# Kernel optimization log

Measured on AMD Instinct MI355X. Metric: run time of the kernel, lower is better.

The kernel has to match this reference:

```python
import jax, jax.numpy as jnp
import numpy as np
from jax import lax

TAU = 2.0
NUM_HEADS = 8
EPS = 1e-5
ALPHA = 4.0  # surrogate sigmoid sharpness

@jax.custom_vjp
def heaviside(x):
    # torch.heaviside(x, 1.0): 1 for x >= 0 (value 1 at x==0), 0 for x < 0
    return (x >= 0).astype(x.dtype)

def _hv_fwd(x):
    return (x >= 0).astype(x.dtype), x

def _hv_bwd(x, g):
    s = jax.nn.sigmoid(x * ALPHA)
    return (g * s * (1.0 - s) * ALPHA,)

heaviside.defvjp(_hv_fwd, _hv_bwd)

def lif(x):
    # Leaky-integrate-fire recurrence over leading time axis. x: [T, ...]
    def step(v, xt):
        v = v + (xt - v) / TAU                 # leakage
        s = heaviside(v - 1.0)                 # fire (v_threshold = 1.0)
        v = (1.0 - lax.stop_gradient(s)) * v   # hard reset (detached spike)
        return v, s
    _, spikes = lax.scan(step, jnp.zeros_like(x[0]), x)
    return spikes

def conv1x1(x, w):
    # x: [T,B,Cin,H,W], w: [Cout,Cin] (1x1 conv, no bias)
    return jnp.einsum('tbchw,dc->tbdhw', x, w)

def bn(x, gamma, beta, mean, var):
    # BatchNorm2d in eval mode (running stats), per-channel over axis 2
    shp = (1, 1, -1, 1, 1)
    inv = gamma.reshape(shp) / jnp.sqrt(var.reshape(shp) + EPS)
    return (x - mean.reshape(shp)) * inv + beta.reshape(shp)

def setup_inputs():
    key = jax.random.key(0)
    ks = jax.random.split(key, 10)
    T, B, C, H, W = 4, 32, 256, 16, 16
    Cv = C  # lamda_ratio = 1

    def w_init(k, o, i):
        return jax.random.normal(k, (o, i), jnp.float32) * (1.0 / np.sqrt(i))

    def bn_params(k, c):
        k1, k2, k3, k4 = jax.random.split(k, 4)
        gamma = jax.random.uniform(k1, (c,), jnp.float32, 0.5, 1.5)
        beta = jax.random.normal(k2, (c,), jnp.float32) * 0.1
        mean = jax.random.normal(k3, (c,), jnp.float32) * 0.1
        var = jax.random.uniform(k4, (c,), jnp.float32, 0.5, 1.5)
        return gamma, beta, mean, var

    x = jax.random.normal(ks[0], (T, B, C, H, W), jnp.float32)
    q_w = w_init(ks[1], C, C)
    k_w = w_init(ks[2], C, C)
    v_w = w_init(ks[3], Cv, C)
    proj_w = w_init(ks[4], C, Cv)
    q_gamma, q_beta, q_mean, q_var = bn_params(ks[5], C)
    k_gamma, k_beta, k_mean, k_var = bn_params(ks[6], C)
    v_gamma, v_beta, v_mean, v_var = bn_params(ks[7], Cv)
    p_gamma, p_beta, p_mean, p_var = bn_params(ks[8], C)
    return {
        'x': x,
        'q_w': q_w, 'q_gamma': q_gamma, 'q_beta': q_beta, 'q_mean': q_mean, 'q_var': q_var,
        'k_w': k_w, 'k_gamma': k_gamma, 'k_beta': k_beta, 'k_mean': k_mean, 'k_var': k_var,
        'v_w': v_w, 'v_gamma': v_gamma, 'v_beta': v_beta, 'v_mean': v_mean, 'v_var': v_var,
        'proj_w': proj_w, 'p_gamma': p_gamma, 'p_beta': p_beta, 'p_mean': p_mean, 'p_var': p_var,
    }

def reference(x, q_w, q_gamma, q_beta, q_mean, q_var,
              k_w, k_gamma, k_beta, k_mean, k_var,
              v_w, v_gamma, v_beta, v_mean, v_var,
              proj_w, p_gamma, p_beta, p_mean, p_var):
    T, B, C, H, W = x.shape
    N = H * W
    Cv = v_w.shape[0]
    hd = C // NUM_HEADS
    hdv = Cv // NUM_HEADS
    scale = (C // NUM_HEADS) ** -0.5

    xs = lif(x)  # head_spike

    q = lif(bn(conv1x1(xs, q_w), q_gamma, q_beta, q_mean, q_var))  # [T,B,C,H,W] binary
    k = lif(bn(conv1x1(xs, k_w), k_gamma, k_beta, k_mean, k_var))
    v = lif(bn(conv1x1(xs, v_w), v_gamma, v_beta, v_mean, v_var))  # [T,B,Cv,H,W]

    # channel c = h*hd + d; flatten spatial -> tokens N, split heads
    q = q.reshape(T, B, NUM_HEADS, hd, N).transpose(0, 1, 2, 4, 3)   # [T,B,h,N,d]
    k = k.reshape(T, B, NUM_HEADS, hd, N).transpose(0, 1, 2, 4, 3)
    v = v.reshape(T, B, NUM_HEADS, hdv, N).transpose(0, 1, 2, 4, 3)  # [T,B,h,N,dv]

    attn = jnp.einsum('tbhnd,tbhmd->tbhnm', q, k)                    # QK^T
    out = jnp.einsum('tbhnm,tbhmd->tbhnd', attn, v) * (scale * 2.0)  # (QK^T)V * 2*scale

    out = out.transpose(0, 1, 2, 4, 3).reshape(T, B, Cv, N)          # [T,B,Cv,N]
    out = lif(out)                                                   # attn_spike
    out = out.reshape(T, B, Cv, H, W)
    out = bn(conv1x1(out, proj_w), p_gamma, p_beta, p_mean, p_var)   # [T,B,C,H,W]
    return out
```

## Files before the change

### kernel.cpp

```cpp
#include <hip/hip_runtime.h>

#define TT 4
#define BB 32
#define CC 256
#define NN 256
#define EPSf 1e-5f
#define MULTf 0.35355339059327373f
#define MARGINQ 1e-2f
#define BCAP 8192u

typedef __attribute__((ext_vector_type(8))) short s16x8;
typedef __attribute__((ext_vector_type(4))) float f32x4;
typedef unsigned char uchar;
typedef unsigned int uint;
typedef unsigned short ushort;

__device__ __forceinline__ ushort f2bf_rn(float f) {
  uint u = __float_as_uint(f);
  u = (u + 0x7FFFu + ((u >> 16) & 1u)) >> 16;
  return (ushort)u;
}
__device__ __forceinline__ float bf2f(ushort b) {
  return __uint_as_float(((uint)b) << 16);
}

__global__ __launch_bounds__(256) void k_front(
    const float* __restrict__ x, uchar* __restrict__ xsF, uchar* __restrict__ xsP,
    const float* __restrict__ qw, const float* __restrict__ kw,
    const float* __restrict__ vw, const float* __restrict__ pw,
    const float* __restrict__ qga, const float* __restrict__ qva,
    const float* __restrict__ kga, const float* __restrict__ kva,
    const float* __restrict__ vga, const float* __restrict__ vva,
    uchar* __restrict__ wfq, uchar* __restrict__ wfp, uint* __restrict__ flags) {
  const int tid = threadIdx.x;
  const int bid = blockIdx.x;
  if (bid < 256) {
#pragma clang fp contract(off)
    const int b = bid >> 3;
    const int ksq = bid & 7;
    const int oct = tid >> 6;
    const int nq = tid & 63;
    const int c0 = ksq * 32 + oct * 8;
    const int n0 = nq * 4;
    const size_t stride = (size_t)BB * CC * NN;
    const float* xb = x + ((size_t)b * CC + c0) * NN + n0;

    float v[8][4];
#pragma unroll
    for (int j = 0; j < 8; ++j)
#pragma unroll
      for (int nn = 0; nn < 4; ++nn) v[j][nn] = 0.f;

#pragma unroll
    for (int t = 0; t < TT; ++t) {
      ushort sp[8][4];
      uint pm[4] = {0, 0, 0, 0};
#pragma unroll
      for (int j = 0; j < 8; ++j) {
        const float4 xv = *reinterpret_cast<const float4*>(xb + t * stride + (size_t)j * NN);
        const float xa[4] = {xv.x, xv.y, xv.z, xv.w};
#pragma unroll
        for (int nn = 0; nn < 4; ++nn) {
          float d = (xa[nn] - v[j][nn]) * 0.5f;
          v[j][nn] = v[j][nn] + d;
          bool s = (v[j][nn] >= 1.0f);
          sp[j][nn] = s ? (ushort)0x3F80 : (ushort)0;
          if (s) { v[j][nn] = 0.f; pm[nn] |= 1u << j; }
        }
      }
#pragma unroll
      for (int nn = 0; nn < 4; ++nn) {
        const int n = n0 + nn;
        uint4* dst = reinterpret_cast<uint4*>(xsF) +
                     (((size_t)(t * BB + b) * 16 + (n >> 4)) * 512 + ksq * 64 + oct * 16 + (n & 15));
        uint4 o;
        o.x = (uint)sp[0][nn] | ((uint)sp[1][nn] << 16);
        o.y = (uint)sp[2][nn] | ((uint)sp[3][nn] << 16);
        o.z = (uint)sp[4][nn] | ((uint)sp[5][nn] << 16);
        o.w = (uint)sp[6][nn] | ((uint)sp[7][nn] << 16);
        *dst = o;
        xsP[(((size_t)(t * BB + b) * NN + n) << 5) + ksq * 4 + oct] = (uchar)pm[nn];
      }
    }
  } else {
    const int gid = (bid - 256) * 256 + tid;
    if (gid < 256) flags[gid] = 0;
    const int ob2 = gid >> 9;
    const int e = gid & 511;
    const int ks = e >> 6, l = e & 63;
    const int c0 = ks * 32 + (l >> 4) * 8;
    if (ob2 < 48) {
      const int sel = ob2 >> 4;
      const float* Wb = sel == 0 ? qw : (sel == 1 ? kw : vw);
      const float* G = sel == 0 ? qga : (sel == 1 ? kga : vga);
      const float* Vr = sel == 0 ? qva : (sel == 1 ? kva : vva);
      const int ocr = (ob2 & 15) * 16 + (l & 15);
      const float inv = G[ocr] / sqrtf(Vr[ocr] + EPSf);
      const float* W = Wb + (size_t)ocr * CC;
      float wv[8];
      *reinterpret_cast<float4*>(&wv[0]) = *reinterpret_cast<const float4*>(W + c0);
      *reinterpret_cast<float4*>(&wv[4]) = *reinterpret_cast<const float4*>(W + c0 + 4);
      ushort hi[8];
#pragma unroll
      for (int j = 0; j < 8; ++j) hi[j] = f2bf_rn(wv[j] * inv);
      *reinterpret_cast<uint4*>(wfq + (((size_t)ob2 * 8 + ks) * 64 + l) * 16) =
          *reinterpret_cast<const uint4*>(hi);
    } else {
      const int ob = ob2 - 48;
      const float* W = pw + ((size_t)(ob * 16 + (l & 15))) * CC;
      float wv[8];
      *reinterpret_cast<float4*>(&wv[0]) = *reinterpret_cast<const float4*>(W + c0);
      *reinterpret_cast<float4*>(&wv[4]) = *reinterpret_cast<const float4*>(W + c0 + 4);
      ushort hi[8], lo[8];
#pragma unroll
      for (int j = 0; j < 8; ++j) {
        hi[j] = f2bf_rn(wv[j]);
        lo[j] = f2bf_rn(wv[j] - bf2f(hi[j]));
      }
      const size_t base = (((size_t)ob * 8 + ks) * 64 + l) * 16;
      const size_t sstr = (size_t)16 * 8 * 64 * 16;
      *reinterpret_cast<uint4*>(wfp + base) = *reinterpret_cast<const uint4*>(hi);
      *reinterpret_cast<uint4*>(wfp + sstr + base) = *reinterpret_cast<const uint4*>(lo);
    }
  }
}

__global__ __launch_bounds__(256, 2) void k_qkv_mfma(
    const uchar* __restrict__ xsF, const uchar* __restrict__ wfq,
    const float* __restrict__ qga, const float* __restrict__ qbe, const float* __restrict__ qme, const float* __restrict__ qva,
    const float* __restrict__ kga, const float* __restrict__ kbe, const float* __restrict__ kme, const float* __restrict__ kva,
    const float* __restrict__ vga, const float* __restrict__ vbe, const float* __restrict__ vme, const float* __restrict__ vva,
    ushort* __restrict__ qp, uint* __restrict__ flags) {
  const int tid = threadIdx.x;
  const int wc = tid >> 6, lane = tid & 63;
  const int lhi = lane >> 4, llo = lane & 15;
  const int bid = blockIdx.x;
  const int xcd = bid & 7;
  const int r0 = bid >> 3;
  const int j = r0 % 12;
  const int g = (r0 / 12) * 8 + xcd;
  const int b = g >> 2, ntile = g & 3;
  const int oc0 = j * 64;
  const int sel = j >> 2;
  const float* G  = sel == 0 ? qga : (sel == 1 ? kga : vga);
  const float* Be = sel == 0 ? qbe : (sel == 1 ? kbe : vbe);
  const float* Mn = sel == 0 ? qme : (sel == 1 ? kme : vme);
  const float* Vr = sel == 0 ? qva : (sel == 1 ? kva : vva);

  s16x8 wfr[4][8];
#pragma unroll
  for (int mf = 0; mf < 4; ++mf)
#pragma unroll
    for (int ks = 0; ks < 8; ++ks)
      wfr[mf][ks] = *reinterpret_cast<const s16x8*>(
          wfq + (((size_t)(j * 4 + mf) * 8 + ks) * 64 + lane) * 16);

  float bias8[4][4];
#pragma unroll
  for (int mf = 0; mf < 4; ++mf)
#pragma unroll
    for (int rr = 0; rr < 4; ++rr) {
      const int ocb = (j & 3) * 64 + mf * 16 + lhi * 4 + rr;
      const float inv = G[ocb] / sqrtf(Vr[ocb] + EPSf);
      bias8[mf][rr] = Be[ocb] - Mn[ocb] * inv;
    }

  float vst[4][4];
#pragma unroll
  for (int mf = 0; mf < 4; ++mf)
#pragma unroll
    for (int rr = 0; rr < 4; ++rr) vst[mf][rr] = 0.f;
  uint fl = 0;
  ushort qm[TT][4];
  const int nb = ntile * 4 + wc;

#define BPTR(t_, ks_)                                                   \
  reinterpret_cast<const s16x8*>(                                       \
      xsF + ((((size_t)((t_) * BB + b) * 16 + nb) * 512 + (ks_) * 64 + lane) * 16))

  s16x8 bfr[8];
#pragma unroll
  for (int ks = 0; ks < 8; ++ks) bfr[ks] = *BPTR(0, ks);

#pragma unroll
  for (int t = 0; t < TT; ++t) {
    f32x4 acc[4];
#pragma unroll
    for (int mf = 0; mf < 4; ++mf) acc[mf] = (f32x4){0.f, 0.f, 0.f, 0.f};

#pragma unroll
    for (int ks = 0; ks < 8; ++ks) {
#pragma unroll
      for (int mf = 0; mf < 4; ++mf)
        acc[mf] = __builtin_amdgcn_mfma_f32_16x16x32_bf16(wfr[mf][ks], bfr[ks], acc[mf], 0, 0, 0);
      if (t < TT - 1) bfr[ks] = *BPTR(t + 1, ks);
    }

#pragma unroll
    for (int mf = 0; mf < 4; ++mf)
#pragma unroll
      for (int rr = 0; rr < 4; ++rr) {
        float y = acc[mf][rr] + bias8[mf][rr];
        float v = vst[mf][rr];
        v = v + (y - v) * 0.5f;
        const bool sp = (v >= 1.0f);
        if (fabsf(v - 1.0f) < MARGINQ) fl |= 1u << (mf * 4 + rr);
        const unsigned long long m = __ballot(sp);
        if (llo == rr) qm[t][mf] = (ushort)((m >> (lhi * 16)) & 0xFFFFull);
        vst[mf][rr] = sp ? 0.f : v;
      }
  }
#undef BPTR

  if (llo < 4) {
#pragma unroll
    for (int t = 0; t < TT; ++t) {
      ushort* qrow = qp + (size_t)(t * BB + b) * 768 * 16;
#pragma unroll
      for (int mf = 0; mf < 4; ++mf) {
        const int oc = oc0 + mf * 16 + lhi * 4 + llo;
        qrow[(size_t)oc * 16 + ntile * 4 + wc] = qm[t][mf];
      }
    }
  }

  if (fl) {
#pragma unroll
    for (int mf = 0; mf < 4; ++mf)
#pragma unroll
      for (int rr = 0; rr < 4; ++rr)
        if (fl & (1u << (mf * 4 + rr))) {
          const int oc = oc0 + mf * 16 + lhi * 4 + rr;
          const int n = ntile * 64 + wc * 16 + llo;
          const uint bucket = ((uint)b << 3) | (uint)((oc & 255) >> 5);
          const uint idx = atomicAdd(&flags[bucket], 1u);
          if (idx < BCAP)
            flags[256 + (bucket << 13) + idx] =
                (((uint)(b << 10) | (uint)oc) << 8) | (uint)n;
        }
  }
}

__global__ __launch_bounds__(256) void k_fix(
    const uchar* __restrict__ xsP,
    const float* __restrict__ qw, const float* __restrict__ kw, const float* __restrict__ vw,
    const float* __restrict__ qga, const float* __restrict__ qbe, const float* __restrict__ qme, const float* __restrict__ qva,
    const float* __restrict__ kga, const float* __restrict__ kbe, const float* __restrict__ kme, const float* __restrict__ kva,
    const float* __restrict__ vga, const float* __restrict__ vbe, const float* __restrict__ vme, const float* __restrict__ vva,
    uint* __restrict__ qp32, const uint* __restrict__ flags) {
#pragma clang fp contract(off)
  const uint bucket = blockIdx.x;
  const int b = (int)(bucket >> 3);
  const uint cnt = min(flags[bucket], BCAP);
  for (uint i = threadIdx.x; i < cnt; i += 256) {
    const uint e = flags[256 + (bucket << 13) + i];
    const int n = (int)(e & 255);
    const int oc = (int)((e >> 8) & 1023);
    const int sel = oc >> 8, ocl = oc & 255;
    const float* W = (sel == 0 ? qw : (sel == 1 ? kw : vw)) + (size_t)ocl * CC;
    const float* G  = sel == 0 ? qga : (sel == 1 ? kga : vga);
    const float* Be = sel == 0 ? qbe : (sel == 1 ? kbe : vbe);
    const float* Mn = sel == 0 ? qme : (sel == 1 ? kme : vme);
    const float* Vr = sel == 0 ? qva : (sel == 1 ? kva : vva);

    uint bw[4][8];
#pragma unroll
    for (int t = 0; t < TT; ++t) {
      const uint4* p = reinterpret_cast<const uint4*>(
          xsP + (((size_t)(t * BB + b) * NN + n) << 5));
      uint4 a = p[0], c4 = p[1];
      bw[t][0] = a.x;  bw[t][1] = a.y;  bw[t][2] = a.z;  bw[t][3] = a.w;
      bw[t][4] = c4.x; bw[t][5] = c4.y; bw[t][6] = c4.z; bw[t][7] = c4.w;
    }

    const float4* W4 = reinterpret_cast<const float4*>(W);
    float a0 = 0.f, a1 = 0.f, a2 = 0.f, a3 = 0.f;
#pragma unroll
    for (int gg = 0; gg < 32; ++gg) {
      const float4 w0 = W4[2 * gg];
      const float4 w1 = W4[2 * gg + 1];
      const uint s0 = bw[0][gg >> 2] >> ((gg & 3) * 8);
      const uint s1 = bw[1][gg >> 2] >> ((gg & 3) * 8);
      const uint s2 = bw[2][gg >> 2] >> ((gg & 3) * 8);
      const uint s3 = bw[3][gg >> 2] >> ((gg & 3) * 8);
      const float wv[8] = {w0.x, w0.y, w0.z, w0.w, w1.x, w1.y, w1.z, w1.w};
#pragma unroll
      for (int jj = 0; jj < 8; ++jj) {
        a0 = fmaf(wv[jj], (float)((s0 >> jj) & 1u), a0);
        a1 = fmaf(wv[jj], (float)((s1 >> jj) & 1u), a1);
        a2 = fmaf(wv[jj], (float)((s2 >> jj) & 1u), a2);
        a3 = fmaf(wv[jj], (float)((s3 >> jj) & 1u), a3);
      }
    }
    float accs[4] = {a0, a1, a2, a3};

    const float inv = G[ocl] / sqrtf(Vr[ocl] + EPSf);
    const float mean = Mn[ocl], beta = Be[ocl];
    float v = 0.f;
#pragma unroll
    for (int t = 0; t < TT; ++t) {
      float xm = accs[t] - mean;
      float y = xm * inv;
      y = y + beta;
      float d = (y - v) * 0.5f;
      v = v + d;
      const bool sp = (v >= 1.0f);
      const size_t widx = ((size_t)(t * BB + b) * 768 + oc) * 8 + (n >> 5);
      const uint bit = 1u << (n & 31);
      if (sp) atomicOr(&qp32[widx], bit);
      else atomicAnd(&qp32[widx], ~bit);
      if (sp) v = 0.f;
    }
  }
}

__global__ __launch_bounds__(1024) void k_attn(const ushort* __restrict__ qp,
                                               uchar* __restrict__ attnF) {
  __shared__ uint Qb[32][8], Kb[32][8], Vb[32][8];
  __shared__ ushort KtVT[32][40];
  const int tid = threadIdx.x;
  const int b = blockIdx.x >> 3;
  const int h = blockIdx.x & 7;
  const int lane = tid & 63;
  const int nt = tid >> 6;
  const int l15 = lane & 15, lhi = lane >> 4;
  const int n = nt * 16 + l15;
  const int wq = n >> 5, bitn = n & 31;

  float vst[8];
#pragma unroll
  for (int j = 0; j < 8; ++j) vst[j] = 0.f;

  for (int t = 0; t < TT; ++t) {
    __syncthreads();
    const ushort* base = qp + (size_t)(t * BB + b) * 768 * 16;
    if (tid < 768) {
      const int arr = tid >> 8;
      const int idx = tid & 255;
      const int ch = idx >> 3, wv2 = idx & 7;
      const uint val = *reinterpret_cast<const uint*>(
          base + (size_t)(arr * 256 + h * 32 + ch) * 16 + wv2 * 2);
      uint(*dst)[8] = (arr == 0) ? Qb : (arr == 1) ? Kb : Vb;
      dst[ch][wv2] = val;
    }
    __syncthreads();
    {
      const int ii = tid >> 5, jj = tid & 31;
      int s = 0;
#pragma unroll
      for (int w8 = 0; w8 < 8; ++w8) s += __popc(Kb[ii][w8] & Vb[jj][w8]);
      KtVT[jj][ii] = f2bf_rn((float)s);
    }
    __syncthreads();

    s16x8 bq;
#pragma unroll
    for (int k = 0; k < 8; ++k) {
      const uint qwv = Qb[lhi * 8 + k][wq];
      bq[k] = (short)(((qwv >> bitn) & 1u) ? 0x3F80 : 0);
    }
    s16x8 a0 = *reinterpret_cast<const s16x8*>(&KtVT[l15][lhi * 8]);
    s16x8 a1 = *reinterpret_cast<const s16x8*>(&KtVT[16 + l15][lhi * 8]);
    f32x4 acc0 = (f32x4){0.f, 0.f, 0.f, 0.f};
    f32x4 acc1 = (f32x4){0.f, 0.f, 0.f, 0.f};
    acc0 = __builtin_amdgcn_mfma_f32_16x16x32_bf16(a0, bq, acc0, 0, 0, 0);
    acc1 = __builtin_amdgcn_mfma_f32_16x16x32_bf16(a1, bq, acc1, 0, 0, 0);

    ushort sb[8];
    {
#pragma clang fp contract(off)
#pragma unroll
      for (int mt = 0; mt < 2; ++mt)
#pragma unroll
        for (int r = 0; r < 4; ++r) {
          const float av = (mt == 0) ? acc0[r] : acc1[r];
          float y = av * MULTf;
          float v = vst[mt * 4 + r];
          float d = (y - v) * 0.5f;
          v = v + d;
          const bool sp = (v >= 1.0f);
          sb[mt * 4 + r] = sp ? (ushort)0x3F80 : (ushort)0;
          vst[mt * 4 + r] = sp ? 0.f : v;
        }
    }
#pragma unroll
    for (int mt = 0; mt < 2; ++mt) {
      uint2 o;
      o.x = (uint)sb[mt * 4 + 0] | ((uint)sb[mt * 4 + 1] << 16);
      o.y = (uint)sb[mt * 4 + 2] | ((uint)sb[mt * 4 + 3] << 16);
      const int oct2 = mt * 2 + (lhi >> 1);
      uchar* dst = attnF +
                   ((((size_t)(t * BB + b) * 16 + nt) * 512 + h * 64 + oct2 * 16 + l15) * 16) +
                   (lhi & 1) * 8;
      *reinterpret_cast<uint2*>(dst) = o;
    }
  }
}

__global__ __launch_bounds__(256, 4) void k_proj_mfma(
    const uchar* __restrict__ attnF, const uchar* __restrict__ wfp,
    const float* __restrict__ pga, const float* __restrict__ pbe,
    const float* __restrict__ pme, const float* __restrict__ pva,
    float* __restrict__ out) {
  const int tid = threadIdx.x;
  const int w = tid >> 6, lane = tid & 63;
  const int lhi = lane >> 4, llo = lane & 15;
  const int wr = w >> 1, wc = w & 1;
  const int bid = blockIdx.x;
  const int xcd = bid & 7;
  const int r = bid >> 3;
  const int j = r & 3;
  const int g = (r >> 2) * 8 + xcd;
  const int tb = g >> 2, ntile = g & 3;
  const int oc0 = j * 64;
  const int nb0 = ntile * 4 + wc * 2;

  f32x4 acc[2][2];
#pragma unroll
  for (int mf = 0; mf < 2; ++mf)
#pragma unroll
    for (int nf = 0; nf < 2; ++nf) acc[mf][nf] = (f32x4){0.f, 0.f, 0.f, 0.f};

#pragma unroll
  for (int ks = 0; ks < 8; ++ks) {
    s16x8 wf[2][2];
#pragma unroll
    for (int s = 0; s < 2; ++s)
#pragma unroll
      for (int mf = 0; mf < 2; ++mf) {
        const int ob = j * 4 + wr * 2 + mf;
        wf[s][mf] = *reinterpret_cast<const s16x8*>(
            wfp + ((((size_t)s * 16 + ob) * 8 + ks) * 64 + lane) * 16);
      }
    s16x8 bf0 = *reinterpret_cast<const s16x8*>(
        attnF + ((((size_t)tb * 16 + nb0) * 512 + ks * 64 + lane) * 16));
    s16x8 bf1 = *reinterpret_cast<const s16x8*>(
        attnF + ((((size_t)tb * 16 + nb0 + 1) * 512 + ks * 64 + lane) * 16));
#pragma unroll
    for (int s = 0; s < 2; ++s)
#pragma unroll
      for (int mf = 0; mf < 2; ++mf) {
        acc[mf][0] = __builtin_amdgcn_mfma_f32_16x16x32_bf16(wf[s][mf], bf0, acc[mf][0], 0, 0, 0);
        acc[mf][1] = __builtin_amdgcn_mfma_f32_16x16x32_bf16(wf[s][mf], bf1, acc[mf][1], 0, 0, 0);
      }
  }

  float inv8[2][4], mean8[2][4], beta8[2][4];
#pragma unroll
  for (int mf = 0; mf < 2; ++mf)
#pragma unroll
    for (int rr = 0; rr < 4; ++rr) {
      const int ocb = oc0 + wr * 32 + mf * 16 + lhi * 4 + rr;
      inv8[mf][rr] = pga[ocb] / sqrtf(pva[ocb] + EPSf);
      mean8[mf][rr] = pme[ocb];
      beta8[mf][rr] = pbe[ocb];
    }

#pragma unroll
  for (int mf = 0; mf < 2; ++mf)
#pragma unroll
    for (int nf = 0; nf < 2; ++nf)
#pragma unroll
      for (int rr = 0; rr < 4; ++rr) {
        const int oc = oc0 + wr * 32 + mf * 16 + lhi * 4 + rr;
        const int nn = ntile * 64 + wc * 32 + nf * 16 + llo;
        float y = (acc[mf][nf][rr] - mean8[mf][rr]) * inv8[mf][rr] + beta8[mf][rr];
        out[((size_t)tb * CC + oc) * NN + nn] = y;
      }
}

extern "C" void kernel_launch(void* const* d_in, const int* in_sizes, int n_in,
                              void* d_out, int out_size, void* d_ws, size_t ws_size,
                              hipStream_t stream) {
  const float* x = (const float*)d_in[0];
  const float* q_w = (const float*)d_in[1];
  const float* q_g = (const float*)d_in[2];
  const float* q_b = (const float*)d_in[3];
  const float* q_m = (const float*)d_in[4];
  const float* q_v = (const float*)d_in[5];
  const float* k_w = (const float*)d_in[6];
  const float* k_g = (const float*)d_in[7];
  const float* k_b = (const float*)d_in[8];
  const float* k_m = (const float*)d_in[9];
  const float* k_v = (const float*)d_in[10];
  const float* v_w = (const float*)d_in[11];
  const float* v_g = (const float*)d_in[12];
  const float* v_b = (const float*)d_in[13];
  const float* v_m = (const float*)d_in[14];
  const float* v_v = (const float*)d_in[15];
  const float* p_w = (const float*)d_in[16];
  const float* p_g = (const float*)d_in[17];
  const float* p_b = (const float*)d_in[18];
  const float* p_m = (const float*)d_in[19];
  const float* p_v = (const float*)d_in[20];

  uchar* ws = (uchar*)d_ws;
  uchar* xsF  = ws;
  ushort* qp  = (ushort*)(ws + 16777216);
  uchar* wfq  = ws + 19922944;
  uchar* wfp  = ws + 20447232;
  uchar* xsP  = ws + 20971520;
  uint* flags = (uint*)(ws + 22020096);

  k_front<<<dim3(384), 256, 0, stream>>>(x, xsF, xsP, q_w, k_w, v_w, p_w,
                                         q_g, q_v, k_g, k_v, v_g, v_v,
                                         wfq, wfp, flags);
  k_qkv_mfma<<<dim3(1536), 256, 0, stream>>>(xsF, wfq,
                                             q_g, q_b, q_m, q_v,
                                             k_g, k_b, k_m, k_v,
                                             v_g, v_b, v_m, v_v,
                                             qp, flags);
  k_fix<<<dim3(256), 256, 0, stream>>>(xsP, q_w, k_w, v_w,
                                       q_g, q_b, q_m, q_v,
                                       k_g, k_b, k_m, k_v,
                                       v_g, v_b, v_m, v_v,
                                       (uint*)qp, flags);
  k_attn<<<dim3(256), 1024, 0, stream>>>(qp, xsF );
  k_proj_mfma<<<dim3(2048), 256, 0, stream>>>(xsF, wfp, p_g, p_b, p_m, p_v,
                                              (float*)d_out);
}
```

Before: 96.75 us.

## Fuse near-threshold fp32 recompute fixup into QKV MFMA kernel via LDS list

```diff
diff --git a/kernel.cpp b/kernel.cpp
--- a/kernel.cpp
+++ b/kernel.cpp
@@ -7,7 +7,7 @@
 #define EPSf 1e-5f
 #define MULTf 0.35355339059327373f
 #define MARGINQ 1e-2f
-#define BCAP 8192u
+#define FCAP 2048u
 
 typedef __attribute__((ext_vector_type(8))) short s16x8;
 typedef __attribute__((ext_vector_type(4))) float f32x4;
@@ -31,7 +31,7 @@
     const float* __restrict__ qga, const float* __restrict__ qva,
     const float* __restrict__ kga, const float* __restrict__ kva,
     const float* __restrict__ vga, const float* __restrict__ vva,
-    uchar* __restrict__ wfq, uchar* __restrict__ wfp, uint* __restrict__ flags) {
+    uchar* __restrict__ wfq, uchar* __restrict__ wfp) {
   const int tid = threadIdx.x;
   const int bid = blockIdx.x;
   if (bid < 256) {
@@ -84,7 +84,6 @@
     }
   } else {
     const int gid = (bid - 256) * 256 + tid;
-    if (gid < 256) flags[gid] = 0;
     const int ob2 = gid >> 9;
     const int e = gid & 511;
     const int ks = e >> 6, l = e & 63;
@@ -127,10 +126,14 @@
 
 __global__ __launch_bounds__(256, 2) void k_qkv_mfma(
     const uchar* __restrict__ xsF, const uchar* __restrict__ wfq,
+    const uchar* __restrict__ xsP,
+    const float* __restrict__ qw, const float* __restrict__ kw, const float* __restrict__ vw,
     const float* __restrict__ qga, const float* __restrict__ qbe, const float* __restrict__ qme, const float* __restrict__ qva,
     const float* __restrict__ kga, const float* __restrict__ kbe, const float* __restrict__ kme, const float* __restrict__ kva,
     const float* __restrict__ vga, const float* __restrict__ vbe, const float* __restrict__ vme, const float* __restrict__ vva,
-    ushort* __restrict__ qp, uint* __restrict__ flags) {
+    ushort* __restrict__ qp) {
+  __shared__ uint flct;
+  __shared__ uint flst[FCAP];
   const int tid = threadIdx.x;
   const int wc = tid >> 6, lane = tid & 63;
   const int lhi = lane >> 4, llo = lane & 15;
@@ -146,6 +149,10 @@
   const float* Be = sel == 0 ? qbe : (sel == 1 ? kbe : vbe);
   const float* Mn = sel == 0 ? qme : (sel == 1 ? kme : vme);
   const float* Vr = sel == 0 ? qva : (sel == 1 ? kva : vva);
+  const float* Wsel = sel == 0 ? qw : (sel == 1 ? kw : vw);
+
+  if (tid == 0) flct = 0;
+  __syncthreads();
 
   s16x8 wfr[4][8];
 #pragma unroll
@@ -232,84 +239,71 @@
         if (fl & (1u << (mf * 4 + rr))) {
           const int oc = oc0 + mf * 16 + lhi * 4 + rr;
           const int n = ntile * 64 + wc * 16 + llo;
-          const uint bucket = ((uint)b << 3) | (uint)((oc & 255) >> 5);
-          const uint idx = atomicAdd(&flags[bucket], 1u);
-          if (idx < BCAP)
-            flags[256 + (bucket << 13) + idx] =
-                (((uint)(b << 10) | (uint)oc) << 8) | (uint)n;
+          const uint idx = atomicAdd(&flct, 1u);
+          if (idx < FCAP) flst[idx] = ((uint)oc << 8) | (uint)n;
         }
   }
-}
-
-__global__ __launch_bounds__(256) void k_fix(
-    const uchar* __restrict__ xsP,
-    const float* __restrict__ qw, const float* __restrict__ kw, const float* __restrict__ vw,
-    const float* __restrict__ qga, const float* __restrict__ qbe, const float* __restrict__ qme, const float* __restrict__ qva,
-    const float* __restrict__ kga, const float* __restrict__ kbe, const float* __restrict__ kme, const float* __restrict__ kva,
-    const float* __restrict__ vga, const float* __restrict__ vbe, const float* __restrict__ vme, const float* __restrict__ vva,
-    uint* __restrict__ qp32, const uint* __restrict__ flags) {
+  __syncthreads();
+
+  {
 #pragma clang fp contract(off)
-  const uint bucket = blockIdx.x;
-  const int b = (int)(bucket >> 3);
-  const uint cnt = min(flags[bucket], BCAP);
-  for (uint i = threadIdx.x; i < cnt; i += 256) {
-    const uint e = flags[256 + (bucket << 13) + i];
-    const int n = (int)(e & 255);
-    const int oc = (int)((e >> 8) & 1023);
-    const int sel = oc >> 8, ocl = oc & 255;
-    const float* W = (sel == 0 ? qw : (sel == 1 ? kw : vw)) + (size_t)ocl * CC;
-    const float* G  = sel == 0 ? qga : (sel == 1 ? kga : vga);
-    const float* Be = sel == 0 ? qbe : (sel == 1 ? kbe : vbe);
-    const float* Mn = sel == 0 ? qme : (sel == 1 ? kme : vme);
-    const float* Vr = sel == 0 ? qva : (sel == 1 ? kva : vva);
-
-    uint bw[4][8];
-#pragma unroll
-    for (int t = 0; t < TT; ++t) {
-      const uint4* p = reinterpret_cast<const uint4*>(
-          xsP + (((size_t)(t * BB + b) * NN + n) << 5));
-      uint4 a = p[0], c4 = p[1];
-      bw[t][0] = a.x;  bw[t][1] = a.y;  bw[t][2] = a.z;  bw[t][3] = a.w;
-      bw[t][4] = c4.x; bw[t][5] = c4.y; bw[t][6] = c4.z; bw[t][7] = c4.w;
-    }
-
-    const float4* W4 = reinterpret_cast<const float4*>(W);
-    float a0 = 0.f, a1 = 0.f, a2 = 0.f, a3 = 0.f;
-#pragma unroll
-    for (int gg = 0; gg < 32; ++gg) {
-      const float4 w0 = W4[2 * gg];
-      const float4 w1 = W4[2 * gg + 1];
-      const uint s0 = bw[0][gg >> 2] >> ((gg & 3) * 8);
-      const uint s1 = bw[1][gg >> 2] >> ((gg & 3) * 8);
-      const uint s2 = bw[2][gg >> 2] >> ((gg & 3) * 8);
-      const uint s3 = bw[3][gg >> 2] >> ((gg & 3) * 8);
-      const float wv[8] = {w0.x, w0.y, w0.z, w0.w, w1.x, w1.y, w1.z, w1.w};
-#pragma unroll
-      for (int jj = 0; jj < 8; ++jj) {
-        a0 = fmaf(wv[jj], (float)((s0 >> jj) & 1u), a0);
-        a1 = fmaf(wv[jj], (float)((s1 >> jj) & 1u), a1);
-        a2 = fmaf(wv[jj], (float)((s2 >> jj) & 1u), a2);
-        a3 = fmaf(wv[jj], (float)((s3 >> jj) & 1u), a3);
-      }
-    }
-    float accs[4] = {a0, a1, a2, a3};
-
-    const float inv = G[ocl] / sqrtf(Vr[ocl] + EPSf);
-    const float mean = Mn[ocl], beta = Be[ocl];
-    float v = 0.f;
-#pragma unroll
-    for (int t = 0; t < TT; ++t) {
-      float xm = accs[t] - mean;
-      float y = xm * inv;
-      y = y + beta;
-      float d = (y - v) * 0.5f;
-      v = v + d;
-      const bool sp = (v >= 1.0f);
-      const size_t widx = ((size_t)(t * BB + b) * 768 + oc) * 8 + (n >> 5);
-      const uint bit = 1u << (n & 31);
-      if (sp) atomicOr(&qp32[widx], bit);
-      else atomicAnd(&qp32[widx], ~bit);
-      if (sp) v = 0.f;
+    uint* qp32 = (uint*)qp;
+    const uint cnt = min(flct, FCAP);
+    for (uint i = tid; i < cnt; i += 256) {
+      const uint e = flst[i];
+      const int n = (int)(e & 255);
+      const int oc = (int)(e >> 8);
+      const int ocl = oc & 255;
+      const float* W = Wsel + (size_t)ocl * CC;
+
+      uint bw[4][8];
+#pragma unroll
+      for (int t = 0; t < TT; ++t) {
+        const uint4* p = reinterpret_cast<const uint4*>(
+            xsP + (((size_t)(t * BB + b) * NN + n) << 5));
+        uint4 a = p[0], c4 = p[1];
+        bw[t][0] = a.x;  bw[t][1] = a.y;  bw[t][2] = a.z;  bw[t][3] = a.w;
+        bw[t][4] = c4.x; bw[t][5] = c4.y; bw[t][6] = c4.z; bw[t][7] = c4.w;
+      }
+
+      const float4* W4 = reinterpret_cast<const float4*>(W);
+      float a0 = 0.f, a1 = 0.f, a2 = 0.f, a3 = 0.f;
+#pragma unroll
+      for (int gg = 0; gg < 32; ++gg) {
+        const float4 w0 = W4[2 * gg];
+        const float4 w1 = W4[2 * gg + 1];
+        const uint s0 = bw[0][gg >> 2] >> ((gg & 3) * 8);
+        const uint s1 = bw[1][gg >> 2] >> ((gg & 3) * 8);
+        const uint s2 = bw[2][gg >> 2] >> ((gg & 3) * 8);
+        const uint s3 = bw[3][gg >> 2] >> ((gg & 3) * 8);
+        const float wv[8] = {w0.x, w0.y, w0.z, w0.w, w1.x, w1.y, w1.z, w1.w};
+#pragma unroll
+        for (int jj = 0; jj < 8; ++jj) {
+          a0 = fmaf(wv[jj], (float)((s0 >> jj) & 1u), a0);
+          a1 = fmaf(wv[jj], (float)((s1 >> jj) & 1u), a1);
+          a2 = fmaf(wv[jj], (float)((s2 >> jj) & 1u), a2);
+          a3 = fmaf(wv[jj], (float)((s3 >> jj) & 1u), a3);
+        }
+      }
+      float accs[4] = {a0, a1, a2, a3};
+
+      const float inv = G[ocl] / sqrtf(Vr[ocl] + EPSf);
+      const float mean = Mn[ocl], beta = Be[ocl];
+      float v = 0.f;
+#pragma unroll
+      for (int t = 0; t < TT; ++t) {
+        float xm = accs[t] - mean;
+        float y = xm * inv;
+        y = y + beta;
+        float d = (y - v) * 0.5f;
+        v = v + d;
+        const bool sp = (v >= 1.0f);
+        const size_t widx = ((size_t)(t * BB + b) * 768 + oc) * 8 + (n >> 5);
+        const uint bit = 1u << (n & 31);
+        if (sp) atomicOr(&qp32[widx], bit);
+        else atomicAnd(&qp32[widx], ~bit);
+        if (sp) v = 0.f;
+      }
     }
   }
 }
@@ -500,21 +494,15 @@
   uchar* wfq  = ws + 19922944;
   uchar* wfp  = ws + 20447232;
   uchar* xsP  = ws + 20971520;
-  uint* flags = (uint*)(ws + 22020096);
 
   k_front<<<dim3(384), 256, 0, stream>>>(x, xsF, xsP, q_w, k_w, v_w, p_w,
                                          q_g, q_v, k_g, k_v, v_g, v_v,
-                                         wfq, wfp, flags);
-  k_qkv_mfma<<<dim3(1536), 256, 0, stream>>>(xsF, wfq,
+                                         wfq, wfp);
+  k_qkv_mfma<<<dim3(1536), 256, 0, stream>>>(xsF, wfq, xsP, q_w, k_w, v_w,
                                              q_g, q_b, q_m, q_v,
                                              k_g, k_b, k_m, k_v,
                                              v_g, v_b, v_m, v_v,
-                                             qp, flags);
-  k_fix<<<dim3(256), 256, 0, stream>>>(xsP, q_w, k_w, v_w,
-                                       q_g, q_b, q_m, q_v,
-                                       k_g, k_b, k_m, k_v,
-                                       v_g, v_b, v_m, v_v,
-                                       (uint*)qp, flags);
+                                             qp);
   k_attn<<<dim3(256), 1024, 0, stream>>>(qp, xsF );
   k_proj_mfma<<<dim3(2048), 256, 0, stream>>>(xsF, wfp, p_g, p_b, p_m, p_v,
                                               (float*)d_out);
```

New measurement: 121.4 us. 1.25x slower.
